# Optimization experiments

Hardware: AMD Instinct MI355X
Metric: run time of the kernel (lower is better)

Reference implementation:

```python
import jax, jax.numpy as jnp
import numpy as np

B, S, D, F, E, NS, K = 2, 2048, 512, 2048, 8, 2, 2


def setup_inputs() -> dict:
    key = jax.random.key(0)
    ks = jax.random.split(key, 6)
    scale = 0.02

    def p(k, shape):
        return jax.random.normal(k, shape, jnp.float32) * scale

    return {
        "x": jax.random.normal(ks[0], (B, S, D), jnp.float32),
        "gate_w": p(ks[1], (E, D)),
        "gate_b": jnp.zeros((E,), jnp.float32),
        "sw1": p(ks[2], (NS, F, D)),
        "sb1": jnp.zeros((NS, F), jnp.float32),
        "sw2": p(ks[3], (NS, D, F)),
        "sb2": jnp.zeros((NS, D), jnp.float32),
        "rw1": p(ks[4], (E, F, D)),
        "rb1": jnp.zeros((E, F), jnp.float32),
        "rw2": p(ks[5], (E, D, F)),
        "rb2": jnp.zeros((E, D), jnp.float32),
    }


def reference(x, gate_w, gate_b, sw1, sb1, sw2, sb2, rw1, rb1, rw2, rb2):
    b, s, d = x.shape
    t = x.reshape(-1, d)  # [T, D] flatten batch*seq tokens
    T = t.shape[0]

    # ---- shared experts: sum over NS FFNs (GELU exact, matching nn.GELU) ----
    hs = jax.nn.gelu(jnp.einsum('td,nfd->ntf', t, sw1) + sb1[:, None, :],
                     approximate=False)
    shared = jnp.einsum('ntf,ndf->td', hs, sw2) + sb2.sum(axis=0)

    # ---- router: softmax over experts, top-k probs/indices ----
    logits = t @ gate_w.T + gate_b               # [T, E]
    probs = jax.nn.softmax(logits, axis=-1)
    top_v, top_i = jax.lax.top_k(probs, K)       # [T, K]

    # combine weights: cw[t, e] = sum_k top_v[t, k] * (top_i[t, k] == e)
    cw = jnp.zeros_like(probs).at[jnp.arange(T)[:, None], top_i].add(top_v)  # [T, E]

    # ---- routed experts: run each expert FFN over all tokens, combine by cw ----
    # Mathematically identical to the masked gather/scatter loop in the source:
    # tokens with cw[t,e]==0 contribute nothing.
    hr = jax.nn.gelu(jnp.einsum('td,efd->etf', t, rw1) + rb1[:, None, :],
                     approximate=False)          # [E, T, F]
    oe = jnp.einsum('etf,edf->etd', hr, rw2) + rb2[:, None, :]  # [E, T, D]
    routed = jnp.einsum('etd,te->td', oe, cw)    # weighted combine

    return (shared + routed).reshape(b, s, d)
```

## Files before the change

### kernel.cpp

```cpp
#include <hip/hip_runtime.h>
#include <math.h>

typedef unsigned short u16;
typedef __attribute__((ext_vector_type(8))) __bf16 bf16x8;
typedef __attribute__((ext_vector_type(4))) float floatx4;

#define T_TOK 4096
#define DD    512
#define FF    2048
#define EE    8
#define NSH   2

#define BM 128
#define BN 128
#define BK 32
#define LDK 40
#define BT2 64
#define CAP 4096
#define PADF 0x80000000u
#define NSLOT (2 * T_TOK + EE * BM)

__device__ __forceinline__ float bf2f(u16 v) {
  union { unsigned int u; float f; } c; c.u = ((unsigned int)v) << 16; return c.f;
}
__device__ __forceinline__ u16 f2bf(float f) {
  union { float ff; unsigned int u; } c; c.ff = f;
  unsigned int u = c.u;
  u += 0x7fffu + ((u >> 16) & 1u);
  return (u16)(u >> 16);
}
__device__ __forceinline__ float decode(const void* p, size_t idx, int f) {
  return f ? ((const float*)p)[idx] : bf2f(((const u16*)p)[idx]);
}
__device__ __forceinline__ bf16x8 load8(const void* base, size_t idx, int f) {
  if (f) {
    const float* p = (const float*)base + idx;
    float4 a = *(const float4*)p;
    float4 b = *(const float4*)(p + 4);
    union { bf16x8 v; u16 s[8]; } u;
    u.s[0] = f2bf(a.x); u.s[1] = f2bf(a.y); u.s[2] = f2bf(a.z); u.s[3] = f2bf(a.w);
    u.s[4] = f2bf(b.x); u.s[5] = f2bf(b.y); u.s[6] = f2bf(b.z); u.s[7] = f2bf(b.w);
    return u.v;
  }
  return *(const bf16x8*)((const u16*)base + idx);
}
__device__ __forceinline__ void loadf8(const void* p, size_t idx, int f,
                                       float* o) {
  if (f) {
    const float* q = (const float*)p + idx;
    float4 a = *(const float4*)q;
    float4 b = *(const float4*)(q + 4);
    o[0] = a.x; o[1] = a.y; o[2] = a.z; o[3] = a.w;
    o[4] = b.x; o[5] = b.y; o[6] = b.z; o[7] = b.w;
  } else {
    union { bf16x8 v; u16 s[8]; } u;
    u.v = *(const bf16x8*)((const u16*)p + idx);
#pragma unroll
    for (int j = 0; j < 8; ++j) o[j] = bf2f(u.s[j]);
  }
}

__device__ __forceinline__ float fast_gelu(float v) {
  float x  = v * 0.70710678118654752f;
  float ax = fabsf(x);
  float t  = __builtin_amdgcn_rcpf(fmaf(0.3275911f, ax, 1.0f));
  float p  = fmaf(t, 1.061405429f, -1.453152027f);
  p = fmaf(t, p, 1.421413741f);
  p = fmaf(t, p, -0.284496736f);
  p = fmaf(t, p, 0.254829592f);
  p = p * t;
  float e  = __expf(-ax * ax);
  float er = fmaf(-p, e, 1.0f);
  er = (x < 0.f) ? -er : er;
  return 0.5f * v * (1.0f + er);
}

__device__ __forceinline__ void gll16(const void* g, void* l) {
  __builtin_amdgcn_global_load_lds(
      (const __attribute__((address_space(1))) void*)g,
      (__attribute__((address_space(3))) void*)l, 16, 0, 0);
}

#define BK2 64
__device__ __forceinline__ void core128swz(
    const u16* gA0, const u16* gA1, const u16* gA2, const u16* gA3,
    const u16* gB0, const u16* gB1, const u16* gB2, const u16* gB3,
    int K, u16* As, u16* Bs, floatx4 acc[4][4],
    int wave, int wm, int wn, int r, int q) {
  const int rs = r & 7;
  for (int k0 = 0; k0 < K; k0 += BK2) {
    __syncthreads();
    gll16(gA0 + k0, As + wave * 512);
    gll16(gA1 + k0, As + 2048 + wave * 512);
    gll16(gA2 + k0, As + 4096 + wave * 512);
    gll16(gA3 + k0, As + 6144 + wave * 512);
    gll16(gB0 + k0, Bs + wave * 512);
    gll16(gB1 + k0, Bs + 2048 + wave * 512);
    gll16(gB2 + k0, Bs + 4096 + wave * 512);
    gll16(gB3 + k0, Bs + 6144 + wave * 512);
    __syncthreads();
#pragma unroll
    for (int s = 0; s < 2; ++s) {
      bf16x8 af[4], bfr[4];
#pragma unroll
      for (int mi = 0; mi < 4; ++mi) {
        int R = wm + mi * 16 + r;
        int u = (s * 4 + q) ^ rs;
        af[mi] = *(const bf16x8*)(As + R * 64 + u * 8);
      }
#pragma unroll
      for (int ni = 0; ni < 4; ++ni) {
        int R = wn + ni * 16 + r;
        int u = (s * 4 + q) ^ rs;
        bfr[ni] = *(const bf16x8*)(Bs + R * 64 + u * 8);
      }
#pragma unroll
      for (int mi = 0; mi < 4; ++mi)
#pragma unroll
        for (int ni = 0; ni < 4; ++ni)
          acc[mi][ni] = __builtin_amdgcn_mfma_f32_16x16x32_bf16(
              af[mi], bfr[ni], acc[mi][ni], 0, 0, 0);
    }
  }
}

__global__ __launch_bounds__(256) void detect_kernel(
    const void* x, const void* gw, const void* sw1, const void* sw2,
    const void* rw1, const void* rw2, int* flags, int* meta) {
  __shared__ int cnt;
  __shared__ int sflags[6];
  const void* ptrs[6] = {x, gw, sw1, sw2, rw1, rw2};
  for (int tnum = 0; tnum < 6; ++tnum) {
    if (threadIdx.x == 0) cnt = 0;
    __syncthreads();
    const u16* p = (const u16*)ptrs[tnum];
    int local = 0;
    for (int i = threadIdx.x; i < 4096; i += 256) {
      unsigned ef = (p[i] >> 7) & 0xFFu;
      if (ef >= 0xE0u) ++local;
    }
    if (local) atomicAdd(&cnt, local);
    __syncthreads();
    if (threadIdx.x == 0) sflags[tnum] = (cnt >= 16) ? 1 : 0;
    __syncthreads();
  }
  if (threadIdx.x == 0) {
#pragma unroll
    for (int i = 0; i < 6; ++i) flags[i] = sflags[i];
    flags[6] = sflags[0];
    flags[7] = 0;
  }
  if (meta && threadIdx.x < 24) meta[threadIdx.x] = 0;
}

#define U8_X  (T_TOK * DD / 8)
#define U8_S1 (NSH * FF * DD / 8)
#define U8_R1 (EE * FF * DD / 8)
#define U8_S2 (NSH * DD * FF / 8)
#define U8_R2 (EE * DD * FF / 8)
#define U8_C0 (U8_X)
#define U8_C1 (U8_C0 + U8_S1)
#define U8_C2 (U8_C1 + U8_R1)
#define U8_C3 (U8_C2 + U8_S2)
#define U8_C4 (U8_C3 + U8_R2)
__global__ __launch_bounds__(256) void conv_all(
    const void* __restrict__ x, const void* __restrict__ sw1,
    const void* __restrict__ rw1, const void* __restrict__ sw2,
    const void* __restrict__ rw2, u16* __restrict__ xb,
    u16* __restrict__ s1b, u16* __restrict__ r1b, u16* __restrict__ s2b,
    u16* __restrict__ r2b, const int* __restrict__ flags) {
  size_t u = (size_t)blockIdx.x * 256 + threadIdx.x;
  const void* src; u16* dst; int fi; size_t base;
  if (u < U8_C0)      { src = x;   dst = xb;  fi = 0; base = 0; }
  else if (u < U8_C1) { src = sw1; dst = s1b; fi = 2; base = U8_C0; }
  else if (u < U8_C2) { src = rw1; dst = r1b; fi = 4; base = U8_C1; }
  else if (u < U8_C3) { src = sw2; dst = s2b; fi = 3; base = U8_C2; }
  else                { src = rw2; dst = r2b; fi = 5; base = U8_C3; }
  int f = flags[fi];
  if (!f) return;
  size_t i = (u - base) * 8;
  *(bf16x8*)(dst + i) = load8(src, i, f);
}

__global__ __launch_bounds__(256) void router_v(
    const void* __restrict__ x, const void* __restrict__ gw,
    const u16* __restrict__ gb, const int* __restrict__ flags,
    float* __restrict__ cw, int2* __restrict__ tix) {
  int wave = threadIdx.x >> 6, lane = threadIdx.x & 63;
  int t = blockIdx.x * 4 + wave;
  int fx = flags[0], fg = flags[1];
  float xf[8];
  loadf8(x, (size_t)t * DD + lane * 8, fx, xf);
  float acc[EE];
#pragma unroll
  for (int e = 0; e < EE; ++e) {
    float gf[8];
    loadf8(gw, (size_t)e * DD + lane * 8, fg, gf);
    float a = 0.f;
#pragma unroll
    for (int j = 0; j < 8; ++j) a = fmaf(xf[j], gf[j], a);
    acc[e] = a;
  }
#pragma unroll
  for (int e = 0; e < EE; ++e) {
    float v = acc[e];
#pragma unroll
    for (int off = 32; off > 0; off >>= 1) v += __shfl_xor(v, off, 64);
    acc[e] = v;
  }
  if (lane == 0) {
    float m = -1e30f;
#pragma unroll
    for (int e = 0; e < EE; ++e) {
      acc[e] += bf2f(gb[e]);
      m = fmaxf(m, acc[e]);
    }
    float p[EE], s = 0.f;
#pragma unroll
    for (int e = 0; e < EE; ++e) { p[e] = expf(acc[e] - m); s += p[e]; }
    int i1 = 0;
#pragma unroll
    for (int e = 1; e < EE; ++e) if (p[e] > p[i1]) i1 = e;
    int i2 = (i1 == 0) ? 1 : 0;
#pragma unroll
    for (int e = 0; e < EE; ++e)
      if (e != i1 && p[e] > p[i2]) i2 = e;
    float inv = 1.0f / s;
#pragma unroll
    for (int e = 0; e < EE; ++e)
      cw[t * EE + e] = (e == i1 || e == i2) ? p[e] * inv : 0.0f;
    tix[t] = make_int2(i1, i2);
  }
}

__global__ __launch_bounds__(1024) void build_pad(
    const int2* __restrict__ tix, int* __restrict__ meta,
    unsigned* __restrict__ list, int4* __restrict__ srec) {
  for (int t = threadIdx.x; t < T_TOK; t += 1024) {
    int2 ii = tix[t];
    int p0 = atomicAdd(&meta[ii.x], 1);
    list[(size_t)ii.x * CAP + p0] = (unsigned)t;
    int p1 = atomicAdd(&meta[ii.y], 1);
    list[(size_t)ii.y * CAP + p1] = (unsigned)t;
    srec[t] = make_int4(ii.x, p0, ii.y, p1);
  }
  __syncthreads();
  if (threadIdx.x == 0) {
    int off = 0;
    for (int e = 0; e < EE; ++e) {
      int c = meta[e];
      int pc = (c + BM - 1) & ~(BM - 1);
      meta[8 + e] = pc;
      meta[16 + e] = off;
      off += pc;
    }
  }
  __syncthreads();
#pragma unroll
  for (int e = 0; e < EE; ++e) {
    int c = meta[e], pc = meta[8 + e];
    for (int i = c + threadIdx.x; i < pc; i += 1024)
      list[(size_t)e * CAP + i] = PADF;
  }
}


__global__ __launch_bounds__(256) void g1_fused(
    const void* __restrict__ xr, const u16* __restrict__ xb,
    const void* __restrict__ s1r, const u16* __restrict__ s1b,
    const u16* __restrict__ sb1,
    const void* __restrict__ r1r, const u16* __restrict__ r1b,
    const u16* __restrict__ rb1, const unsigned* __restrict__ list,
    const int* __restrict__ meta, const int* __restrict__ flags,
    u16* __restrict__ Hsh, u16* __restrict__ Hrt) {
  const u16* xp  = flags[0] ? xb  : (const u16*)xr;
  const u16* s1p = flags[2] ? s1b : (const u16*)s1r;
  const u16* r1p = flags[4] ? r1b : (const u16*)r1r;

  int L  = blockIdx.x + 16 * (blockIdx.y + 32 * blockIdx.z);
  int xx = (L & 127) >> 3;
  int pp = ((L >> 7) << 3) | (L & 7);
  int z  = pp >> 5;
  int bm = (pp & 31) * BM;

  int tid = threadIdx.x, lane = tid & 63, wave = tid >> 6;
  int wm = (wave >> 1) * 64, wn = (wave & 1) * 64;
  int r = lane & 15, q = lane >> 4;
  const int K = DD;

  int rsub = tid >> 3;
  int us = (tid & 7) ^ (rsub & 7);

  __shared__ u16 As[BM * BK2];
  __shared__ u16 Bs[BN * BK2];

  const u16 *gA[4], *gB[4];
  int e = 0, ho = 0, bn;
  if (z < 2) {
    bn = (z * 16 + xx) * BN;
#pragma unroll
    for (int c = 0; c < 4; ++c) {
      gA[c] = xp + (size_t)(bm + c * 32 + rsub) * K + us * 8;
      gB[c] = s1p + (size_t)(bn + c * 32 + rsub) * K + us * 8;
    }
  } else {
    e = z - 2;
    if (bm >= meta[8 + e]) return;
    ho = meta[16 + e];
    bn = xx * BN;
#pragma unroll
    for (int c = 0; c < 4; ++c) {
      unsigned tk = list[(size_t)e * CAP + bm + c * 32 + rsub] & 0x7fffffffu;
      gA[c] = xp + (size_t)tk * K + us * 8;
      gB[c] = r1p + (size_t)e * FF * DD + (size_t)(bn + c * 32 + rsub) * K +
              us * 8;
    }
  }

  floatx4 acc[4][4];
  floatx4 zero = {0.f, 0.f, 0.f, 0.f};
#pragma unroll
  for (int i = 0; i < 4; ++i)
#pragma unroll
    for (int j = 0; j < 4; ++j) acc[i][j] = zero;

  core128swz(gA[0], gA[1], gA[2], gA[3], gB[0], gB[1], gB[2], gB[3],
             K, As, Bs, acc, wave, wm, wn, r, q);

  if (z < 2) {
#pragma unroll
    for (int mi = 0; mi < 4; ++mi)
#pragma unroll
      for (int ni = 0; ni < 4; ++ni) {
        int col = bn + wn + ni * 16 + r;
        float bv = bf2f(sb1[col]);
#pragma unroll
        for (int rr = 0; rr < 4; ++rr) {
          int row = bm + wm + mi * 16 + q * 4 + rr;
          float v = acc[mi][ni][rr] + bv;
          Hsh[(size_t)row * (NSH * FF) + col] = f2bf(fast_gelu(v));
        }
      }
  } else {
#pragma unroll
    for (int mi = 0; mi < 4; ++mi)
#pragma unroll
      for (int ni = 0; ni < 4; ++ni) {
        int col = bn + wn + ni * 16 + r;
        float bv = bf2f(rb1[(size_t)e * FF + col]);
#pragma unroll
        for (int rr = 0; rr < 4; ++rr) {
          int slot = bm + wm + mi * 16 + q * 4 + rr;
          float v = acc[mi][ni][rr] + bv;
          Hrt[(size_t)(ho + slot) * FF + col] = f2bf(fast_gelu(v));
        }
      }
  }
}

__global__ __launch_bounds__(256) void g2_fused(
    const u16* __restrict__ Hsh,
    const void* __restrict__ s2r, const u16* __restrict__ s2b,
    const u16* __restrict__ sb2, const u16* __restrict__ Hrt,
    const void* __restrict__ r2r, const u16* __restrict__ r2b,
    const u16* __restrict__ rb2,
    const unsigned* __restrict__ list, const int* __restrict__ meta,
    const int* __restrict__ flags, const float* __restrict__ cw,
    float* __restrict__ oacc, float* __restrict__ Ort) {
  const u16* s2p = flags[3] ? s2b : (const u16*)s2r;
  const u16* r2p = flags[5] ? r2b : (const u16*)r2r;

  int L  = blockIdx.x + 4 * (blockIdx.y + 32 * blockIdx.z);
  int xx = (L & 31) >> 3;
  int pp = ((L >> 5) << 3) | (L & 7);
  int z  = pp >> 5;
  int bm = (pp & 31) * BM;
  int bn = xx * BN;

  int tid = threadIdx.x, lane = tid & 63, wave = tid >> 6;
  int wm = (wave >> 1) * 64, wn = (wave & 1) * 64;
  int r = lane & 15, q = lane >> 4;
  const int K = FF;

  int rsub = tid >> 3;
  int us = (tid & 7) ^ (rsub & 7);

  __shared__ u16 As[BM * BK2];
  __shared__ u16 Bs[BN * BK2];

  const u16 *gA[4], *gB[4];
  int e = 0, ho = 0;
  if (z < NSH) {
    const int ldA = NSH * FF;
#pragma unroll
    for (int c = 0; c < 4; ++c) {
      gA[c] = Hsh + (size_t)(bm + c * 32 + rsub) * ldA + (size_t)z * FF +
              us * 8;
      gB[c] = s2p + (size_t)z * DD * FF + (size_t)(bn + c * 32 + rsub) * K +
              us * 8;
    }
  } else {
    e = z - NSH;
    if (bm >= meta[8 + e]) return;
    ho = meta[16 + e];
#pragma unroll
    for (int c = 0; c < 4; ++c) {
      gA[c] = Hrt + (size_t)(ho + bm + c * 32 + rsub) * K + us * 8;
      gB[c] = r2p + (size_t)e * DD * FF + (size_t)(bn + c * 32 + rsub) * K +
              us * 8;
    }
  }

  floatx4 acc[4][4];
  floatx4 zero = {0.f, 0.f, 0.f, 0.f};
#pragma unroll
  for (int i = 0; i < 4; ++i)
#pragma unroll
    for (int j = 0; j < 4; ++j) acc[i][j] = zero;

  core128swz(gA[0], gA[1], gA[2], gA[3], gB[0], gB[1], gB[2], gB[3],
             K, As, Bs, acc, wave, wm, wn, r, q);

  if (z < NSH) {
    float* op = oacc + (size_t)z * T_TOK * DD;
#pragma unroll
    for (int mi = 0; mi < 4; ++mi)
#pragma unroll
      for (int ni = 0; ni < 4; ++ni) {
        int col = bn + wn + ni * 16 + r;
        float bv = bf2f(sb2[(size_t)z * DD + col]);
#pragma unroll
        for (int rr = 0; rr < 4; ++rr) {
          int row = bm + wm + mi * 16 + q * 4 + rr;
          op[(size_t)row * DD + col] = acc[mi][ni][rr] + bv;
        }
      }
  } else {
#pragma unroll
    for (int mi = 0; mi < 4; ++mi)
#pragma unroll
      for (int rr = 0; rr < 4; ++rr) {
        int slot = bm + wm + mi * 16 + q * 4 + rr;
        unsigned raw = list[(size_t)e * CAP + slot];
        if (raw & PADF) continue;
        float s = cw[raw * EE + e];
#pragma unroll
        for (int ni = 0; ni < 4; ++ni) {
          int col = bn + wn + ni * 16 + r;
          float v = acc[mi][ni][rr] + bf2f(rb2[(size_t)e * DD + col]);
          Ort[(size_t)(ho + slot) * DD + col] = s * v;
        }
      }
  }
}

typedef struct { u16 a, b, c, d; } u16x4;
__global__ __launch_bounds__(256) void combine_out(
    const float* __restrict__ oacc, const float* __restrict__ Ort,
    const int4* __restrict__ srec, const int* __restrict__ meta,
    void* __restrict__ out, const int* __restrict__ flags) {
  int t  = blockIdx.x * 2 + (threadIdx.x >> 7);
  int c4 = (threadIdx.x & 127) * 4;
  int4 sr = srec[t];
  int g0 = meta[16 + sr.x] + sr.y;
  int g1 = meta[16 + sr.z] + sr.w;
  float4 a = *(const float4*)(oacc + (size_t)t * DD + c4);
  float4 b = *(const float4*)(oacc + (size_t)(T_TOK + t) * DD + c4);
  float4 u = *(const float4*)(Ort + (size_t)g0 * DD + c4);
  float4 v = *(const float4*)(Ort + (size_t)g1 * DD + c4);
  float o0 = a.x + b.x + u.x + v.x;
  float o1 = a.y + b.y + u.y + v.y;
  float o2 = a.z + b.z + u.z + v.z;
  float o3 = a.w + b.w + u.w + v.w;
  size_t idx = (size_t)t * DD + c4;
  if (flags[6]) {
    *(float4*)((float*)out + idx) = make_float4(o0, o1, o2, o3);
  } else {
    u16x4 h = {f2bf(o0), f2bf(o1), f2bf(o2), f2bf(o3)};
    *(u16x4*)((u16*)out + idx) = h;
  }
}

__device__ __forceinline__ void gemm_core(const void* A, size_t aoff, int fA,
                                          const void* B, size_t boff, int fB,
                                          int K, u16* As, u16* Bs,
                                          floatx4 acc[4][4]) {
  int tid  = threadIdx.x;
  int lane = tid & 63, wave = tid >> 6;
  int wm = (wave >> 1) * 64, wn = (wave & 1) * 64;
  int r = lane & 15, q = lane >> 4;
  int srow = tid >> 2;
  int sc8  = (tid & 3) * 8;
  size_t abase = aoff + (size_t)srow * K + sc8;
  size_t bbase = boff + (size_t)srow * K + sc8;
  const size_t half = (size_t)64 * K;

  for (int k0 = 0; k0 < K; k0 += BK) {
    bf16x8 av0 = load8(A, abase + k0, fA);
    bf16x8 av1 = load8(A, abase + half + k0, fA);
    bf16x8 bv0 = load8(B, bbase + k0, fB);
    bf16x8 bv1 = load8(B, bbase + half + k0, fB);
    __syncthreads();
    *(bf16x8*)(As + srow * LDK + sc8)        = av0;
    *(bf16x8*)(As + (srow + 64) * LDK + sc8) = av1;
    *(bf16x8*)(Bs + srow * LDK + sc8)        = bv0;
    *(bf16x8*)(Bs + (srow + 64) * LDK + sc8) = bv1;
    __syncthreads();

    bf16x8 af[4], bfr[4];
#pragma unroll
    for (int mi = 0; mi < 4; ++mi)
      af[mi] = *(const bf16x8*)(As + (wm + mi * 16 + r) * LDK + q * 8);
#pragma unroll
    for (int ni = 0; ni < 4; ++ni)
      bfr[ni] = *(const bf16x8*)(Bs + (wn + ni * 16 + r) * LDK + q * 8);
#pragma unroll
    for (int mi = 0; mi < 4; ++mi)
#pragma unroll
      for (int ni = 0; ni < 4; ++ni)
        acc[mi][ni] = __builtin_amdgcn_mfma_f32_16x16x32_bf16(
            af[mi], bfr[ni], acc[mi][ni], 0, 0, 0);
  }
}

__global__ __launch_bounds__(256) void gemm1_gelu(
    const void* __restrict__ A, size_t aoff, const void* __restrict__ B,
    size_t boff, const u16* __restrict__ bias, size_t bioff,
    u16* __restrict__ H, const int* __restrict__ flags, int iA, int iB,
    int N, int K) {
  __shared__ u16 As[BM * LDK];
  __shared__ u16 Bs[BN * LDK];
  int fA = flags[iA], fB = flags[iB];
  floatx4 acc[4][4];
  floatx4 zero = {0.f, 0.f, 0.f, 0.f};
#pragma unroll
  for (int i = 0; i < 4; ++i)
#pragma unroll
    for (int j = 0; j < 4; ++j) acc[i][j] = zero;

  int bm = blockIdx.y * BM, bn = blockIdx.x * BN;
  gemm_core(A, aoff + (size_t)bm * K, fA, B, boff + (size_t)bn * K, fB, K,
            As, Bs, acc);

  int tid = threadIdx.x, wave = tid >> 6, lane = tid & 63;
  int wm = (wave >> 1) * 64, wn = (wave & 1) * 64;
  int r = lane & 15, q = lane >> 4;
#pragma unroll
  for (int mi = 0; mi < 4; ++mi)
#pragma unroll
    for (int ni = 0; ni < 4; ++ni) {
      int col = bn + wn + ni * 16 + r;
      float bv = bf2f(bias[bioff + col]);
#pragma unroll
      for (int rr = 0; rr < 4; ++rr) {
        int row = bm + wm + mi * 16 + q * 4 + rr;
        float v = acc[mi][ni][rr] + bv;
        H[(size_t)row * N + col] = f2bf(fast_gelu(v));
      }
    }
}

__global__ __launch_bounds__(256) void gemm2_acc(
    const u16* __restrict__ A, const void* __restrict__ B, size_t boff,
    const u16* __restrict__ bias, size_t bioff, float* __restrict__ outf,
    void* __restrict__ outb, const float* __restrict__ cw,
    const int* __restrict__ flags, int iB, int expert, int accum,
    int row0, int N, int K) {
  __shared__ u16 As[BT2 * LDK];
  __shared__ u16 Bs[BT2 * LDK];
  int fB = flags[iB], fO = flags[6];
  floatx4 acc[2][2];
  floatx4 zero = {0.f, 0.f, 0.f, 0.f};
#pragma unroll
  for (int i = 0; i < 2; ++i)
#pragma unroll
    for (int j = 0; j < 2; ++j) acc[i][j] = zero;

  int bm = blockIdx.y * BT2, bn = blockIdx.x * BT2;
  int tid  = threadIdx.x;
  int lane = tid & 63, wave = tid >> 6;
  int wm = (wave >> 1) * 32, wn = (wave & 1) * 32;
  int r = lane & 15, q = lane >> 4;
  int srow = tid >> 2;
  int sc8  = (tid & 3) * 8;
  size_t abase = (size_t)(bm + srow) * K + sc8;
  size_t bbase = boff + (size_t)(bn + srow) * K + sc8;

  for (int k0 = 0; k0 < K; k0 += BK) {
    bf16x8 av = *(const bf16x8*)(A + abase + k0);
    bf16x8 bv = load8(B, bbase + k0, fB);
    __syncthreads();
    *(bf16x8*)(As + srow * LDK + sc8) = av;
    *(bf16x8*)(Bs + srow * LDK + sc8) = bv;
    __syncthreads();

    bf16x8 af[2], bfr[2];
#pragma unroll
    for (int mi = 0; mi < 2; ++mi)
      af[mi] = *(const bf16x8*)(As + (wm + mi * 16 + r) * LDK + q * 8);
#pragma unroll
    for (int ni = 0; ni < 2; ++ni)
      bfr[ni] = *(const bf16x8*)(Bs + (wn + ni * 16 + r) * LDK + q * 8);
#pragma unroll
    for (int mi = 0; mi < 2; ++mi)
#pragma unroll
      for (int ni = 0; ni < 2; ++ni)
        acc[mi][ni] = __builtin_amdgcn_mfma_f32_16x16x32_bf16(
            af[mi], bfr[ni], acc[mi][ni], 0, 0, 0);
  }

#pragma unroll
  for (int mi = 0; mi < 2; ++mi)
#pragma unroll
    for (int rr = 0; rr < 4; ++rr) {
      int grow = row0 + bm + wm + mi * 16 + q * 4 + rr;
      float s = cw ? cw[grow * EE + expert] : 1.0f;
#pragma unroll
      for (int ni = 0; ni < 2; ++ni) {
        int col = bn + wn + ni * 16 + r;
        float v = acc[mi][ni][rr] + bf2f(bias[bioff + col]);
        size_t idx = (size_t)grow * N + col;
        if (outf) {
          float prev = accum ? outf[idx] : 0.0f;
          outf[idx] = prev + s * v;
        } else if (fO) {
          float* ob = (float*)outb;
          float prev = accum ? ob[idx] : 0.0f;
          ob[idx] = prev + s * v;
        } else {
          u16* ob = (u16*)outb;
          float prev = accum ? bf2f(ob[idx]) : 0.0f;
          ob[idx] = f2bf(prev + s * v);
        }
      }
    }
}

__global__ __launch_bounds__(256) void convert_out(
    const float* __restrict__ acc, void* __restrict__ out,
    const int* __restrict__ flags, int n) {
  int i = blockIdx.x * blockDim.x + threadIdx.x;
  if (i >= n) return;
  if (flags[6]) ((float*)out)[i] = acc[i];
  else ((u16*)out)[i] = f2bf(acc[i]);
}

extern "C" void kernel_launch(void* const* d_in, const int* in_sizes, int n_in,
                              void* d_out, int out_size, void* d_ws, size_t ws_size,
                              hipStream_t stream) {
  (void)in_sizes; (void)n_in; (void)out_size;
  const void* x   = d_in[0];
  const void* gw  = d_in[1];
  const u16*  gb  = (const u16*)d_in[2];
  const void* sw1 = d_in[3];
  const u16*  sb1 = (const u16*)d_in[4];
  const void* sw2 = d_in[5];
  const u16*  sb2 = (const u16*)d_in[6];
  const void* rw1 = d_in[7];
  const u16*  rb1 = (const u16*)d_in[8];
  const void* rw2 = d_in[9];
  const u16*  rb2 = (const u16*)d_in[10];

  const size_t NX   = (size_t)T_TOK * DD;
  const size_t NW1S = (size_t)NSH * FF * DD;
  const size_t NW1R = (size_t)EE * FF * DD;
  const size_t NW2S = (size_t)NSH * DD * FF;
  const size_t NW2R = (size_t)EE * DD * FF;

  size_t off = 0;
  const size_t flO   = off; off += 256;
  const size_t cwO   = off; off += (size_t)T_TOK * EE * 4;
  const size_t tixO  = off; off += (size_t)T_TOK * 8;
  const size_t metaO = off; off += 256;
  const size_t listO = off; off += (size_t)EE * CAP * 4;
  const size_t srecO = off; off += (size_t)T_TOK * 16;
  const size_t accO  = off; off += (size_t)NSH * T_TOK * DD * 4;
  const size_t hshO  = off; off += (size_t)T_TOK * NSH * FF * 2;
  const size_t hrtO  = off; off += (size_t)NSLOT * FF * 2;
  const size_t ortO  = off; off += (size_t)NSLOT * DD * 4;
  const size_t xbO   = off; off += NX * 2;
  const size_t s1O   = off; off += NW1S * 2;
  const size_t r1O   = off; off += NW1R * 2;
  const size_t s2O   = off; off += NW2S * 2;
  const size_t r2O   = off; off += NW2R * 2;
  const int fast = (off <= ws_size) ? 1 : 0;

  char* ws = (char*)d_ws;
  int*   flags = (int*)(ws + flO);
  float* cw    = (float*)(ws + cwO);
  dim3 blk(256);

  if (fast) {
    int2*     tix  = (int2*)(ws + tixO);
    int*      meta = (int*)(ws + metaO);
    unsigned* list = (unsigned*)(ws + listO);
    int4*     srec = (int4*)(ws + srecO);
    float*    oacc = (float*)(ws + accO);
    u16*      Hsh  = (u16*)(ws + hshO);
    u16*      Hrt  = (u16*)(ws + hrtO);
    float*    Ort  = (float*)(ws + ortO);
    u16*      xb   = (u16*)(ws + xbO);
    u16*      s1b  = (u16*)(ws + s1O);
    u16*      r1b  = (u16*)(ws + r1O);
    u16*      s2b  = (u16*)(ws + s2O);
    u16*      r2b  = (u16*)(ws + r2O);

    detect_kernel<<<1, 256, 0, stream>>>(x, gw, sw1, sw2, rw1, rw2, flags,
                                         meta);
    conv_all<<<U8_C4 / 256, 256, 0, stream>>>(x, sw1, rw1, sw2, rw2, xb, s1b,
                                              r1b, s2b, r2b, flags);
    router_v<<<T_TOK / 4, 256, 0, stream>>>(x, gw, gb, flags, cw, tix);
    build_pad<<<1, 1024, 0, stream>>>(tix, meta, list, srec);

    dim3 gf1(16, T_TOK / BM, 2 + EE);
    g1_fused<<<gf1, blk, 0, stream>>>(x, xb, sw1, s1b, sb1, rw1, r1b, rb1,
                                      list, meta, flags, Hsh, Hrt);
    dim3 gf2(DD / BN, CAP / BM, NSH + EE);
    g2_fused<<<gf2, blk, 0, stream>>>(Hsh, sw2, s2b, sb2, Hrt, rw2, r2b, rb2,
                                      list, meta, flags, cw, oacc, Ort);
    combine_out<<<T_TOK / 2, 256, 0, stream>>>(oacc, Ort, srec, meta, d_out,
                                               flags);
    return;
  }

  detect_kernel<<<1, 256, 0, stream>>>(x, gw, sw1, sw2, rw1, rw2, flags,
                                       nullptr);
  const size_t flB = 256, cwB = (size_t)T_TOK * EE * 4, tixB = (size_t)T_TOK * 8;
  const size_t accB = (size_t)T_TOK * DD * 4;
  static const int tcs[4] = {4096, 2048, 1024, 512};
  int TC = 0, use_f32 = 1;
  for (int i = 0; i < 4; ++i)
    if (flB + cwB + tixB + accB + (size_t)tcs[i] * FF * 2 <= ws_size) { TC = tcs[i]; break; }
  if (!TC) {
    use_f32 = 0;
    for (int i = 0; i < 4; ++i)
      if (flB + cwB + tixB + (size_t)tcs[i] * FF * 2 <= ws_size) { TC = tcs[i]; break; }
  }
  if (!TC) { TC = 512; use_f32 = 0; }

  int2*  tix     = (int2*)(ws + flB + cwB);
  float* out_acc = use_f32 ? (float*)(ws + flB + cwB + tixB) : nullptr;
  u16*   H       = (u16*)(ws + flB + cwB + tixB + (use_f32 ? accB : 0));

  router_v<<<T_TOK / 4, 256, 0, stream>>>(x, gw, gb, flags, cw, tix);
  dim3 g1(FF / BN, TC / BM);
  dim3 g2(DD / BT2, TC / BT2);
  const int nchunk = T_TOK / TC;
  for (int f = 0; f < NSH + EE; ++f) {
    const void *w1, *w2; const u16 *b1, *b2; const float* cwp;
    int expert, i1, i2v; size_t w1off, w2off, b1off, b2off;
    if (f < NSH) {
      w1 = sw1; w2 = sw2; b1 = sb1; b2 = sb2;
      w1off = (size_t)f * FF * DD; w2off = (size_t)f * DD * FF;
      b1off = (size_t)f * FF; b2off = (size_t)f * DD;
      cwp = nullptr; expert = 0; i1 = 2; i2v = 3;
    } else {
      int e = f - NSH;
      w1 = rw1; w2 = rw2; b1 = rb1; b2 = rb2;
      w1off = (size_t)e * FF * DD; w2off = (size_t)e * DD * FF;
      b1off = (size_t)e * FF; b2off = (size_t)e * DD;
      cwp = cw; expert = e; i1 = 4; i2v = 5;
    }
    int accum = (f > 0) ? 1 : 0;
    for (int c = 0; c < nchunk; ++c) {
      size_t t0 = (size_t)c * TC;
      gemm1_gelu<<<g1, blk, 0, stream>>>(x, t0 * DD, w1, w1off, b1, b1off, H,
                                         flags, 0, i1, FF, DD);
      gemm2_acc<<<g2, blk, 0, stream>>>(H, w2, w2off, b2, b2off, out_acc,
                                        d_out, cwp, flags, i2v, expert, accum,
                                        (int)t0, DD, FF);
    }
  }
  if (use_f32)
    convert_out<<<(T_TOK * DD) / 256, 256, 0, stream>>>(out_acc, d_out, flags,
                                                        T_TOK * DD);
}
```

Baseline: 374.7 us.

## Double-buffer LDS tiles in MoE GEMM core to overlap loads with MFMA

Replaces the single-buffered GEMM mainloop with a two-stage LDS pipeline. The next K-tile is issued via global_load_lds before computing on the current one, with explicit vmcnt waits and barriers. This hides global-to-LDS latency behind the MFMA work, at the cost of doubling LDS per block (32KB to 64KB), which may reduce occupancy. It also drops the swizzled block-index remapping in g1_fused in favour of direct grid indexing, which can change L2 locality.

```diff
diff --git a/kernel.cpp b/kernel.cpp
--- a/kernel.cpp
+++ b/kernel.cpp
@@ -82,23 +82,43 @@
 }
 
 #define BK2 64
-__device__ __forceinline__ void core128swz(
+#define TILEU (BM * BK2)
+
+__device__ __forceinline__ void stage8(
+    const u16* gA0, const u16* gA1, const u16* gA2, const u16* gA3,
+    const u16* gB0, const u16* gB1, const u16* gB2, const u16* gB3,
+    u16* Asb, u16* Bsb, int wave, int k0) {
+  gll16(gA0 + k0, Asb + wave * 512);
+  gll16(gA1 + k0, Asb + 2048 + wave * 512);
+  gll16(gA2 + k0, Asb + 4096 + wave * 512);
+  gll16(gA3 + k0, Asb + 6144 + wave * 512);
+  gll16(gB0 + k0, Bsb + wave * 512);
+  gll16(gB1 + k0, Bsb + 2048 + wave * 512);
+  gll16(gB2 + k0, Bsb + 4096 + wave * 512);
+  gll16(gB3 + k0, Bsb + 6144 + wave * 512);
+}
+
+__device__ __forceinline__ void core128pipe(
     const u16* gA0, const u16* gA1, const u16* gA2, const u16* gA3,
     const u16* gB0, const u16* gB1, const u16* gB2, const u16* gB3,
     int K, u16* As, u16* Bs, floatx4 acc[4][4],
     int wave, int wm, int wn, int r, int q) {
   const int rs = r & 7;
+  stage8(gA0, gA1, gA2, gA3, gB0, gB1, gB2, gB3, As, Bs, wave, 0);
+  int cur = 0;
   for (int k0 = 0; k0 < K; k0 += BK2) {
-    __syncthreads();
-    gll16(gA0 + k0, As + wave * 512);
-    gll16(gA1 + k0, As + 2048 + wave * 512);
-    gll16(gA2 + k0, As + 4096 + wave * 512);
-    gll16(gA3 + k0, As + 6144 + wave * 512);
-    gll16(gB0 + k0, Bs + wave * 512);
-    gll16(gB1 + k0, Bs + 2048 + wave * 512);
-    gll16(gB2 + k0, Bs + 4096 + wave * 512);
-    gll16(gB3 + k0, Bs + 6144 + wave * 512);
-    __syncthreads();
+    const u16* Ac = As + cur * TILEU;
+    const u16* Bc = Bs + cur * TILEU;
+    if (k0 + BK2 < K) {
+      stage8(gA0, gA1, gA2, gA3, gB0, gB1, gB2, gB3,
+             As + (cur ^ 1) * TILEU, Bs + (cur ^ 1) * TILEU, wave, k0 + BK2);
+      asm volatile("s_waitcnt vmcnt(8)" ::: "memory");
+    } else {
+      asm volatile("s_waitcnt vmcnt(0)" ::: "memory");
+    }
+    __builtin_amdgcn_sched_barrier(0);
+    __builtin_amdgcn_s_barrier();
+    __builtin_amdgcn_sched_barrier(0);
 #pragma unroll
     for (int s = 0; s < 2; ++s) {
       bf16x8 af[4], bfr[4];
@@ -106,13 +126,13 @@
       for (int mi = 0; mi < 4; ++mi) {
         int R = wm + mi * 16 + r;
         int u = (s * 4 + q) ^ rs;
-        af[mi] = *(const bf16x8*)(As + R * 64 + u * 8);
+        af[mi] = *(const bf16x8*)(Ac + R * 64 + u * 8);
       }
 #pragma unroll
       for (int ni = 0; ni < 4; ++ni) {
         int R = wn + ni * 16 + r;
         int u = (s * 4 + q) ^ rs;
-        bfr[ni] = *(const bf16x8*)(Bs + R * 64 + u * 8);
+        bfr[ni] = *(const bf16x8*)(Bc + R * 64 + u * 8);
       }
 #pragma unroll
       for (int mi = 0; mi < 4; ++mi)
@@ -121,6 +141,9 @@
           acc[mi][ni] = __builtin_amdgcn_mfma_f32_16x16x32_bf16(
               af[mi], bfr[ni], acc[mi][ni], 0, 0, 0);
     }
+    __builtin_amdgcn_sched_barrier(0);
+    __builtin_amdgcn_s_barrier();
+    cur ^= 1;
   }
 }
 
@@ -277,11 +300,9 @@
   const u16* s1p = flags[2] ? s1b : (const u16*)s1r;
   const u16* r1p = flags[4] ? r1b : (const u16*)r1r;
 
-  int L  = blockIdx.x + 16 * (blockIdx.y + 32 * blockIdx.z);
-  int xx = (L & 127) >> 3;
-  int pp = ((L >> 7) << 3) | (L & 7);
-  int z  = pp >> 5;
-  int bm = (pp & 31) * BM;
+  int z  = blockIdx.z;
+  int bm = blockIdx.y * BM;
+  int xx = blockIdx.x;
 
   int tid = threadIdx.x, lane = tid & 63, wave = tid >> 6;
   int wm = (wave >> 1) * 64, wn = (wave & 1) * 64;
@@ -291,8 +312,8 @@
   int rsub = tid >> 3;
   int us = (tid & 7) ^ (rsub & 7);
 
-  __shared__ u16 As[BM * BK2];
-  __shared__ u16 Bs[BN * BK2];
+  __shared__ u16 As[2 * TILEU];
+  __shared__ u16 Bs[2 * TILEU];
 
   const u16 *gA[4], *gB[4];
   int e = 0, ho = 0, bn;
@@ -324,8 +345,8 @@
 #pragma unroll
     for (int j = 0; j < 4; ++j) acc[i][j] = zero;
 
-  core128swz(gA[0], gA[1], gA[2], gA[3], gB[0], gB[1], gB[2], gB[3],
-             K, As, Bs, acc, wave, wm, wn, r, q);
+  core128pipe(gA[0], gA[1], gA[2], gA[3], gB[0], gB[1], gB[2], gB[3],
+              K, As, Bs, acc, wave, wm, wn, r, q);
 
   if (z < 2) {
 #pragma unroll
@@ -385,8 +406,8 @@
   int rsub = tid >> 3;
   int us = (tid & 7) ^ (rsub & 7);
 
-  __shared__ u16 As[BM * BK2];
-  __shared__ u16 Bs[BN * BK2];
+  __shared__ u16 As[2 * TILEU];
+  __shared__ u16 Bs[2 * TILEU];
 
   const u16 *gA[4], *gB[4];
   int e = 0, ho = 0;
@@ -418,8 +439,8 @@
 #pragma unroll
     for (int j = 0; j < 4; ++j) acc[i][j] = zero;
 
-  core128swz(gA[0], gA[1], gA[2], gA[3], gB[0], gB[1], gB[2], gB[3],
-             K, As, Bs, acc, wave, wm, wn, r, q);
+  core128pipe(gA[0], gA[1], gA[2], gA[3], gB[0], gB[1], gB[2], gB[3],
+              K, As, Bs, acc, wave, wm, wn, r, q);
 
   if (z < NSH) {
     float* op = oacc + (size_t)z * T_TOK * DD;
```

Measured after the change: 369.8 us. Within noise of the previous version (-1.3%).
